# Kernel optimization log

Measured on AMD Instinct MI355X. Metric: run time of the kernel, lower is better.

Reference implementation:

```python
import jax, jax.numpy as jnp
import numpy as np

EPS = 1e-5
H, D = 8, 64  # n_heads, head_n_channels


def _instance_norm(x):
    # x: [B, H, N, D]; InstanceNorm1d over grid axis N per (batch, head, channel)
    m = jnp.mean(x, axis=2, keepdims=True)
    v = jnp.var(x, axis=2, keepdims=True)
    return (x - m) * jax.lax.rsqrt(v + EPS)


def setup_inputs() -> dict:
    key = jax.random.key(0)
    ks = jax.random.split(key, 7)
    B, N, C, OUT = 4, 16384, 256, 256
    u_src = jax.random.normal(ks[0], (B, N, C), jnp.float32)
    pos_src = jax.random.uniform(ks[1], (B, N, 2), jnp.float32)
    s_in = 1.0 / np.sqrt(C)
    Wq = jax.random.normal(ks[2], (H * D, C), jnp.float32) * s_in
    Wk = jax.random.normal(ks[3], (H * D, C), jnp.float32) * s_in
    Wv = jax.random.normal(ks[4], (H * D, C), jnp.float32) * s_in
    Wo = jax.random.normal(ks[5], (OUT, H * D), jnp.float32) * (1.0 / np.sqrt(H * D))
    bo = jnp.zeros((OUT,), jnp.float32)
    return {"u_src": u_src, "pos_src": pos_src, "Wq": Wq, "Wk": Wk, "Wv": Wv, "Wo": Wo, "bo": bo}


def reference(u_src, pos_src, Wq, Wk, Wv, Wo, bo):
    B, N, C = u_src.shape
    # q/k/v projections -> [B, H, N, D]
    q = (u_src @ Wq.T).reshape(B, N, H, D).transpose(0, 2, 1, 3)
    k = (u_src @ Wk.T).reshape(B, N, H, D).transpose(0, 2, 1, 3)
    v = (u_src @ Wv.T).reshape(B, N, H, D).transpose(0, 2, 1, 3)
    # instance-norm k, v over the grid (domain) axis
    k = _instance_norm(k)
    v = _instance_norm(v)
    # associative linear attention with uniform quadrature weights 1/N
    w = 1.0 / N
    kv = jnp.einsum('bhnd,bhne->bhde', k, v * w)   # [B,H,D,D]
    u = jnp.einsum('bhnd,bhde->bhne', q, kv)       # [B,H,N,D]
    u = u.transpose(0, 2, 1, 3).reshape(B, N, H * D)
    return u @ Wo.T + bo
```

## Files before the change

kernel.cpp:

```cpp
#include <hip/hip_runtime.h>
#include <hip/hip_bf16.h>

#define BB    4
#define NTOT  16384
#define CC    256
#define HH    8
#define DD    64
#define HD    512
#define OUTC  256

typedef unsigned short u16;
typedef unsigned int u32;
typedef __attribute__((ext_vector_type(8))) short bf16x8;
typedef __attribute__((ext_vector_type(4))) float f32x4;
typedef __attribute__((ext_vector_type(4))) short u16x4;
typedef __attribute__((ext_vector_type(4))) u32 u32x4;

__device__ __forceinline__ float b2f(u16 u) {
    union { float f; u32 i; } x; x.i = ((u32)u) << 16; return x.f;
}
__device__ __forceinline__ u16 f2b(float f) {
    union { float f; u32 i; } x; x.f = f;
    u32 r = x.i + 0x7fffu + ((x.i >> 16) & 1u);
    return (u16)(r >> 16);
}

#define GLD(gp, lp) __builtin_amdgcn_global_load_lds( \
    (const __attribute__((address_space(1))) void*)(gp), \
    (__attribute__((address_space(3))) void*)(lp), 16, 0, 0)

#define MFMA(a, b, c) __builtin_amdgcn_mfma_f32_16x16x32_bf16((a), (b), (c), 0, 0, 0)

__global__ __launch_bounds__(256) void wcvt(
    const float* __restrict__ Wq, const float* __restrict__ Wk,
    const float* __restrict__ Wv, const float* __restrict__ Wo,
    u16* __restrict__ q, u16* __restrict__ k,
    u16* __restrict__ v, u16* __restrict__ o)
{
    const int z = blockIdx.z;
    const float* src = z == 0 ? Wq : z == 1 ? Wk : z == 2 ? Wv : Wo;
    u16* dst = z == 0 ? q : z == 1 ? k : z == 2 ? v : o;
    const int i = (blockIdx.x * 256 + threadIdx.x) * 8;
    const float4 a = *(const float4*)(src + i);
    const float4 b = *(const float4*)(src + i + 4);
    union { bf16x8 v; u16 s[8]; } w;
    w.s[0] = f2b(a.x); w.s[1] = f2b(a.y); w.s[2] = f2b(a.z); w.s[3] = f2b(a.w);
    w.s[4] = f2b(b.x); w.s[5] = f2b(b.y); w.s[6] = f2b(b.z); w.s[7] = f2b(b.w);
    *(bf16x8*)(dst + i) = w.v;
}

__global__ __launch_bounds__(512) void ggemm(
    const float* __restrict__ u, float* __restrict__ Gp, float* __restrict__ suP,
    u16* __restrict__ u_b)
{
    __shared__ u32 Ts[16 * 290];
    const int z = blockIdx.x, b = z >> 6, ck = z & 63;
    const float* base = u + (long long)b * NTOT * CC + (long long)ck * 256 * CC;
    u16* ub_base = u_b + (long long)b * NTOT * CC + (long long)ck * 256 * CC;
    const int t = threadIdx.x, w = t >> 6, l = t & 63;
    const int wy = w >> 1, wx = w & 1;
    const int r16 = l & 15, quad = l >> 4;
    const int sp = t >> 5;
    const int sq = t & 31;

    const int csa0 = 9 * ((wy * 64 + r16) >> 3) + (r16 & 7);
    const int csb0 = 9 * ((wx * 128 + r16) >> 3) + (r16 & 7);
    const int pr0 = 4 * quad * 290;

    f32x4 acc[4][8] = {};
    float su = 0.f;

    float4 a0, a1, b0, b1;
    {
        const float* src = base + (long long)(2 * sp) * CC + sq * 8;
        a0 = *(const float4*)src;       a1 = *(const float4*)(src + 4);
        b0 = *(const float4*)(src + CC); b1 = *(const float4*)(src + CC + 4);
    }

    for (int it = 0; it < 8; it++) {
        __syncthreads();
        {
            union { bf16x8 v; u16 q[8]; } ra, rb;
            ra.q[0] = f2b(a0.x); ra.q[1] = f2b(a0.y); ra.q[2] = f2b(a0.z); ra.q[3] = f2b(a0.w);
            ra.q[4] = f2b(a1.x); ra.q[5] = f2b(a1.y); ra.q[6] = f2b(a1.z); ra.q[7] = f2b(a1.w);
            rb.q[0] = f2b(b0.x); rb.q[1] = f2b(b0.y); rb.q[2] = f2b(b0.z); rb.q[3] = f2b(b0.w);
            rb.q[4] = f2b(b1.x); rb.q[5] = f2b(b1.y); rb.q[6] = f2b(b1.z); rb.q[7] = f2b(b1.w);
            {
                u16* ub = ub_base + (long long)(it * 32 + 2 * sp) * CC + sq * 8;
                *(bf16x8*)ub = ra.v;
                *(bf16x8*)(ub + CC) = rb.v;
            }
            u32 pk[8];
#pragma unroll
            for (int k = 0; k < 8; k++)
                pk[k] = (u32)ra.q[k] | ((u32)rb.q[k] << 16);
            u32* dst = Ts + sp * 290 + 9 * sq;
#pragma unroll
            for (int k = 0; k < 8; k++) dst[k] = pk[k];
        }
        if (it < 7) {
            const float* src = base + (long long)((it + 1) * 32 + 2 * sp) * CC + sq * 8;
            a0 = *(const float4*)src;       a1 = *(const float4*)(src + 4);
            b0 = *(const float4*)(src + CC); b1 = *(const float4*)(src + CC + 4);
        }
        __syncthreads();

        if (t < 256) {
            const int cs = 9 * (t >> 3) + (t & 7);
            float s1 = 0.f;
#pragma unroll
            for (int p = 0; p < 16; p++) {
                u32 v = Ts[p * 290 + cs];
                s1 += b2f((u16)(v & 0xffff)) + b2f((u16)(v >> 16));
            }
            su += s1;
        }

        bf16x8 a[4], bb[8];
#pragma unroll
        for (int i = 0; i < 4; i++) {
            const int cs = csa0 + 18 * i;
            union { u32x4 u4; bf16x8 h; } f;
            f.u4[0] = Ts[pr0 + cs];       f.u4[1] = Ts[pr0 + 290 + cs];
            f.u4[2] = Ts[pr0 + 580 + cs]; f.u4[3] = Ts[pr0 + 870 + cs];
            a[i] = f.h;
        }
#pragma unroll
        for (int j = 0; j < 8; j++) {
            const int cs = csb0 + 18 * j;
            union { u32x4 u4; bf16x8 h; } f;
            f.u4[0] = Ts[pr0 + cs];       f.u4[1] = Ts[pr0 + 290 + cs];
            f.u4[2] = Ts[pr0 + 580 + cs]; f.u4[3] = Ts[pr0 + 870 + cs];
            bb[j] = f.h;
        }
#pragma unroll
        for (int i = 0; i < 4; i++)
#pragma unroll
            for (int j = 0; j < 8; j++)
                acc[i][j] = MFMA(a[i], bb[j], acc[i][j]);
    }

    float* Cp = Gp + (long long)z * 65536;
#pragma unroll
    for (int i = 0; i < 4; i++)
#pragma unroll
        for (int j = 0; j < 8; j++)
#pragma unroll
            for (int rr = 0; rr < 4; rr++)
                Cp[(wy * 64 + 16 * i + quad * 4 + rr) * 256 + wx * 128 + 16 * j + r16]
                    = acc[i][j][rr];
    if (t < 256) suP[z * 256 + t] = su;
}

__global__ __launch_bounds__(256) void gred(
    const float* __restrict__ Gp, const float* __restrict__ suP,
    u16* __restrict__ Gb, float* __restrict__ su)
{
    const int b = blockIdx.y, t = threadIdx.x;
    const int row = blockIdx.x * 4 + (t >> 6);
    const int col = (t & 63) * 4;
    const float* p = Gp + (long long)(b * 64) * 65536 + row * 256 + col;
    f32x4 s = {};
#pragma unroll
    for (int ck = 0; ck < 64; ck++) {
        f32x4 v = *(const f32x4*)(p + (long long)ck * 65536);
        s[0] += v[0]; s[1] += v[1]; s[2] += v[2]; s[3] += v[3];
    }
    union { u16x4 v; u16 q[4]; } pk;
#pragma unroll
    for (int k = 0; k < 4; k++) pk.q[k] = f2b(s[k]);
    *(u16x4*)(Gb + (long long)b * 65536 + row * 256 + col) = pk.v;

    if (blockIdx.x == 0) {
        float s2 = 0.f;
#pragma unroll
        for (int ck = 0; ck < 64; ck++) s2 += suP[(b * 64 + ck) * 256 + t];
        su[b * 256 + t] = s2;
    }
}

__global__ __launch_bounds__(256) void skvz(
    const u16* __restrict__ P2, const float* __restrict__ su,
    const u16* __restrict__ Wk_b, const u16* __restrict__ Wv_b,
    const u16* __restrict__ Wq_b, u16* __restrict__ Zt)
{
    __shared__ u16 pool[20480];
    __shared__ float mkL[64], rkL[64], mvL[64], rvL[64];

    const int bx = blockIdx.x, b = bx >> 3, h = bx & 7;
    const int t = threadIdx.x, w = t >> 6, l = t & 63;
    const int r16 = l & 15, quad = l >> 4;

    const u16* WkH = Wk_b + (h * 64) * 256;
    const u16* WvH = Wv_b + (h * 64) * 256;
    const u16* PkH = P2 + (long long)b * 262144 + (h * 64) * 256;
    const u16* PvH = P2 + (long long)b * 262144 + (512 + h * 64) * 256;

    {
        const int row = t >> 1, half = t & 1;
        const u16* Prow = (row < 64 ? PkH + row * 256 : PvH + (row - 64) * 256) + half * 128;
        const u16* Wrow = (row < 64 ? WkH + row * 256 : WvH + (row - 64) * 256) + half * 128;
        const float* suB = su + b * 256 + half * 128;
        float e2 = 0.f, m = 0.f;
#pragma unroll
        for (int c8 = 0; c8 < 16; c8++) {
            bf16x8 pw = *(const bf16x8*)(Prow + c8 * 8);
            bf16x8 ww = *(const bf16x8*)(Wrow + c8 * 8);
#pragma unroll
            for (int k = 0; k < 8; k++) {
                const float wv_ = b2f((u16)ww[k]);
                e2 += b2f((u16)pw[k]) * wv_;
                m  += wv_ * suB[c8 * 8 + k];
            }
        }
        e2 += __shfl_xor(e2, 1);
        m  += __shfl_xor(m, 1);
        if (half == 0) {
            m *= (1.0f / NTOT);
            const float r = rsqrtf(e2 * (1.0f / NTOT) - m * m + 1e-5f);
            if (row < 64) { mkL[row] = m; rkL[row] = r; }
            else          { mvL[row - 64] = m; rvL[row - 64] = r; }
        }
    }
    __syncthreads();

    const int mh = (w >> 1) * 32, nh = (w & 1) * 32;
    float mkR[2][4], rkR[2][4], mvR[2], rvR[2];
#pragma unroll
    for (int i = 0; i < 2; i++)
#pragma unroll
        for (int rr = 0; rr < 4; rr++) {
            mkR[i][rr] = mkL[mh + 16 * i + quad * 4 + rr];
            rkR[i][rr] = rkL[mh + 16 * i + quad * 4 + rr];
        }
#pragma unroll
    for (int j = 0; j < 2; j++) {
        mvR[j] = mvL[nh + 16 * j + r16];
        rvR[j] = rvL[nh + 16 * j + r16];
    }

    f32x4 accs[2][2] = {};
    for (int ch = 0; ch < 8; ch++) {
        const int ko = quad * 8;
        bf16x8 ap[2], bv[2];
#pragma unroll
        for (int i = 0; i < 2; i++)
            ap[i] = *(const bf16x8*)(PkH + (mh + 16 * i + r16) * 256 + ch * 32 + ko);
#pragma unroll
        for (int j = 0; j < 2; j++)
            bv[j] = *(const bf16x8*)(WvH + (nh + 16 * j + r16) * 256 + ch * 32 + ko);
#pragma unroll
        for (int i = 0; i < 2; i++)
#pragma unroll
            for (int j = 0; j < 2; j++)
                accs[i][j] = MFMA(ap[i], bv[j], accs[i][j]);
    }

    u16* kvTL = pool;
    u16* WqTL = pool + 4096;
#pragma unroll
    for (int i = 0; i < 2; i++)
#pragma unroll
        for (int j = 0; j < 2; j++)
#pragma unroll
            for (int rr = 0; rr < 4; rr++) {
                const int d = mh + 16 * i + quad * 4 + rr;
                const int e = nh + 16 * j + r16;
                const float kv = rkR[i][rr] * rvR[j] *
                    (accs[i][j][rr] * (1.0f / NTOT) - mkR[i][rr] * mvR[j]);
                kvTL[(d >> 5) * 2048 + e * 32 + (d & 31)] = f2b(kv);
            }
    {
        const int d = t >> 2, q = t & 3;
        const u16* Wrow = Wq_b + (h * 64 + d) * 256 + q * 64;
#pragma unroll
        for (int s = 0; s < 8; s++) {
            bf16x8 raw = *(const bf16x8*)(Wrow + s * 8);
#pragma unroll
            for (int k = 0; k < 8; k++) {
                const int c = q * 64 + s * 8 + k;
                WqTL[(d >> 5) * 8192 + c * 32 + (d & 31)] = (u16)raw[k];
            }
        }
    }
    __syncthreads();

    f32x4 accy[4][4] = {};
#pragma unroll
    for (int ch = 0; ch < 2; ch++) {
        const int ko = quad * 8;
        bf16x8 akv[4], bq[4];
#pragma unroll
        for (int i = 0; i < 4; i++)
            akv[i] = *(const bf16x8*)(kvTL + ch * 2048 + (16 * i + r16) * 32 + ko);
#pragma unroll
        for (int j = 0; j < 4; j++)
            bq[j] = *(const bf16x8*)(WqTL + ch * 8192 + (w * 64 + 16 * j + r16) * 32 + ko);
#pragma unroll
        for (int i = 0; i < 4; i++)
#pragma unroll
            for (int j = 0; j < 4; j++)
                accy[i][j] = MFMA(akv[i], bq[j], accy[i][j]);
    }
#pragma unroll
    for (int i = 0; i < 4; i++)
#pragma unroll
        for (int j = 0; j < 4; j++) {
            const int c = w * 64 + 16 * j + r16;
            const int e0 = 16 * i + quad * 4;
            union { u16x4 v; u16 s[4]; } pk;
#pragma unroll
            for (int rr = 0; rr < 4; rr++) pk.s[rr] = f2b(accy[i][j][rr]);
            *(u16x4*)(Zt + ((long long)(b * 256 + c)) * 512 + h * 64 + e0) = pk.v;
        }
}

template <typename CT>
__global__ __launch_bounds__(256) void gemm_bt(
    const u16* __restrict__ A, const u16* __restrict__ Bm,
    CT* __restrict__ C, const float* __restrict__ bias,
    int K, int lda, int ldc,
    long long aStride, long long bStride, long long cStride)
{
    __shared__ u16 As[128 * 32];
    __shared__ u16 Bs[128 * 32];

    const int bz = blockIdx.z;
    A  += (long long)bz * aStride;
    Bm += (long long)bz * bStride;
    C  += (long long)bz * cStride;

    const int m0 = blockIdx.x * 128;
    const int n0 = blockIdx.y * 128;
    const int t  = threadIdx.x;
    const int wv = t >> 6, l = t & 63;
    const int wy = wv >> 1, wx = wv & 1;
    const int r16  = l & 15;
    const int quad = l >> 4;
    const int srow = wv * 16 + (l >> 2);
    const int scol = (l & 3) * 8;

    f32x4 acc[4][4] = {};

    for (int kk = 0; kk < K; kk += 32) {
#pragma unroll
        for (int s = 0; s < 2; s++) {
            GLD(A + (long long)(m0 + s * 64 + srow) * lda + kk + scol,
                As + s * 2048 + wv * 512);
            GLD(Bm + (long long)(n0 + s * 64 + srow) * K + kk + scol,
                Bs + s * 2048 + wv * 512);
        }
        __syncthreads();

        bf16x8 a[4], b[4];
#pragma unroll
        for (int i = 0; i < 4; i++)
            a[i] = *(const bf16x8*)(As + (wy * 64 + 16 * i + r16) * 32 + quad * 8);
#pragma unroll
        for (int j = 0; j < 4; j++)
            b[j] = *(const bf16x8*)(Bs + (wx * 64 + 16 * j + r16) * 32 + quad * 8);
#pragma unroll
        for (int i = 0; i < 4; i++)
#pragma unroll
            for (int j = 0; j < 4; j++)
                acc[i][j] = MFMA(a[i], b[j], acc[i][j]);
        __syncthreads();
    }

#pragma unroll
    for (int j = 0; j < 4; j++) {
        const int col = n0 + wx * 64 + 16 * j + r16;
        const float bv = bias ? bias[col] : 0.0f;
#pragma unroll
        for (int i = 0; i < 4; i++) {
#pragma unroll
            for (int r = 0; r < 4; r++) {
                const int row = m0 + wy * 64 + 16 * i + quad * 4 + r;
                const float v = acc[i][j][r] + bv;
                if constexpr (sizeof(CT) == 2) C[(long long)row * ldc + col] = f2b(v);
                else                           C[(long long)row * ldc + col] = v;
            }
        }
    }
}

__global__ __launch_bounds__(256) void gemm_out(
    const u16* __restrict__ Au, const u16* __restrict__ Ft,
    float* __restrict__ C, const float* __restrict__ bias)
{
    __shared__ u16 As[128 * 32];
    __shared__ u16 Bs[256 * 32];

    const int b = blockIdx.z;
    Au += (long long)b * NTOT * CC;
    const u16* Bm = Ft + (long long)b * 65536;
    C += (long long)b * NTOT * OUTC;

    const int m0 = blockIdx.x * 128;
    const int t  = threadIdx.x;
    const int wv = t >> 6, l = t & 63;
    const int wy = wv >> 1, wx = wv & 1;
    const int r16  = l & 15;
    const int quad = l >> 4;
    const int srow = wv * 16 + (l >> 2);
    const int scol = (l & 3) * 8;

    f32x4 acc[4][8] = {};

    for (int kk = 0; kk < 256; kk += 32) {
#pragma unroll
        for (int s = 0; s < 2; s++)
            GLD(Au + (long long)(m0 + s * 64 + srow) * CC + kk + scol,
                As + s * 2048 + wv * 512);
#pragma unroll
        for (int s = 0; s < 4; s++)
            GLD(Bm + (long long)(s * 64 + srow) * 256 + kk + scol,
                Bs + s * 2048 + wv * 512);
        __syncthreads();

        bf16x8 a[4], bb[8];
#pragma unroll
        for (int i = 0; i < 4; i++)
            a[i] = *(const bf16x8*)(As + (wy * 64 + 16 * i + r16) * 32 + quad * 8);
#pragma unroll
        for (int j = 0; j < 8; j++)
            bb[j] = *(const bf16x8*)(Bs + (wx * 128 + 16 * j + r16) * 32 + quad * 8);
#pragma unroll
        for (int i = 0; i < 4; i++)
#pragma unroll
            for (int j = 0; j < 8; j++)
                acc[i][j] = MFMA(a[i], bb[j], acc[i][j]);
        __syncthreads();
    }

#pragma unroll
    for (int j = 0; j < 8; j++) {
        const int col = wx * 128 + 16 * j + r16;
        const float bv = bias[col];
#pragma unroll
        for (int i = 0; i < 4; i++) {
#pragma unroll
            for (int r = 0; r < 4; r++) {
                const int row = m0 + wy * 64 + 16 * i + quad * 4 + r;
                C[(long long)row * OUTC + col] = acc[i][j][r] + bv;
            }
        }
    }
}

extern "C" void kernel_launch(void* const* d_in, const int* in_sizes, int n_in,
                              void* d_out, int out_size, void* d_ws, size_t ws_size,
                              hipStream_t stream)
{
    const float* u_src = (const float*)d_in[0];
    const float* Wq = (const float*)d_in[2];
    const float* Wk = (const float*)d_in[3];
    const float* Wv = (const float*)d_in[4];
    const float* Wo = (const float*)d_in[5];
    const float* bo = (const float*)d_in[6];
    float* out = (float*)d_out;

    char* ws = (char*)d_ws;
    size_t off = 0;
    float* Gp  = (float*)(ws + off); off += 67108864;
    float* suP = (float*)(ws + off); off += 262144;
    u16*  Gb   = (u16*)(ws + off);  off += 524288;
    u16*  Wq_b = (u16*)(ws + off);  off += 262144;
    u16*  Wk_b = (u16*)(ws + off);  off += 262144;
    u16*  Wv_b = (u16*)(ws + off);  off += 262144;
    u16*  Wo_b = (u16*)(ws + off);  off += 262144;
    float* su  = (float*)(ws + off); off += 4096;
    u16*  Zt   = (u16*)(ws + off);  off += 1048576;
    u16*  Ft   = (u16*)(ws + off);  off += 524288;
    u16*  P2   = (u16*)(ws + off);  off += 2097152;
    u16*  u_b  = (u16*)(ws + off);  off += 33554432;

    const dim3 blk(256);

    wcvt<<<dim3(64, 1, 4), blk, 0, stream>>>(Wq, Wk, Wv, Wo, Wq_b, Wk_b, Wv_b, Wo_b);

    ggemm<<<dim3(BB * 64), dim3(512), 0, stream>>>(u_src, Gp, suP, u_b);
    gred<<<dim3(64, BB), blk, 0, stream>>>(Gp, suP, Gb, su);

    gemm_bt<u16><<<dim3(8, 2, BB), blk, 0, stream>>>(
        Wk_b, Gb, P2, nullptr, 256, 256, 256, 0, 65536, 262144);

    skvz<<<dim3(BB * HH), blk, 0, stream>>>(P2, su, Wk_b, Wv_b, Wq_b, Zt);

    gemm_bt<u16><<<dim3(2, 2, BB), blk, 0, stream>>>(
        Wo_b, Zt, Ft, nullptr, 512, 512, 256, 0, 131072, 65536);

    gemm_out<<<dim3(128, 1, BB), blk, 0, stream>>>(u_b, Ft, out, bo);
}
```

Before: 214.3 us.

## Double-buffer shared memory in GEMM kernels and move column sums to registers

Adds ping-pong LDS buffers to ggemm, gemm_bt and gemm_out so the next K-tile's global-to-LDS load is issued before the current tile's MFMAs. This drops one barrier per iteration and overlaps load latency with compute. In ggemm, the per-column sum is now accumulated in registers during bf16 conversion and reduced once through LDS at the end, replacing a per-iteration LDS sweep by half the threads. The cost is doubled LDS per block, which may lower occupancy.

```diff
diff --git a/kernel.cpp b/kernel.cpp
--- a/kernel.cpp
+++ b/kernel.cpp
@@ -53,7 +53,7 @@
     const float* __restrict__ u, float* __restrict__ Gp, float* __restrict__ suP,
     u16* __restrict__ u_b)
 {
-    __shared__ u32 Ts[16 * 290];
+    __shared__ u32 Ts[2 * 4640];
     const int z = blockIdx.x, b = z >> 6, ck = z & 63;
     const float* base = u + (long long)b * NTOT * CC + (long long)ck * 256 * CC;
     u16* ub_base = u_b + (long long)b * NTOT * CC + (long long)ck * 256 * CC;
@@ -68,7 +68,7 @@
     const int pr0 = 4 * quad * 290;
 
     f32x4 acc[4][8] = {};
-    float su = 0.f;
+    float su8[8] = {};
 
     float4 a0, a1, b0, b1;
     {
@@ -77,60 +77,54 @@
         b0 = *(const float4*)(src + CC); b1 = *(const float4*)(src + CC + 4);
     }
 
+    int cur = 0;
     for (int it = 0; it < 8; it++) {
-        __syncthreads();
+        const u32 coff = cur * 4640;
         {
             union { bf16x8 v; u16 q[8]; } ra, rb;
             ra.q[0] = f2b(a0.x); ra.q[1] = f2b(a0.y); ra.q[2] = f2b(a0.z); ra.q[3] = f2b(a0.w);
             ra.q[4] = f2b(a1.x); ra.q[5] = f2b(a1.y); ra.q[6] = f2b(a1.z); ra.q[7] = f2b(a1.w);
             rb.q[0] = f2b(b0.x); rb.q[1] = f2b(b0.y); rb.q[2] = f2b(b0.z); rb.q[3] = f2b(b0.w);
             rb.q[4] = f2b(b1.x); rb.q[5] = f2b(b1.y); rb.q[6] = f2b(b1.z); rb.q[7] = f2b(b1.w);
+#pragma unroll
+            for (int k = 0; k < 8; k++)
+                su8[k] += b2f(ra.q[k]) + b2f(rb.q[k]);
+            u32 pk[8];
+#pragma unroll
+            for (int k = 0; k < 8; k++)
+                pk[k] = (u32)ra.q[k] | ((u32)rb.q[k] << 16);
+            u32* dst = Ts + coff + sp * 290 + 9 * sq;
+#pragma unroll
+            for (int k = 0; k < 8; k++) dst[k] = pk[k];
             {
                 u16* ub = ub_base + (long long)(it * 32 + 2 * sp) * CC + sq * 8;
                 *(bf16x8*)ub = ra.v;
                 *(bf16x8*)(ub + CC) = rb.v;
             }
-            u32 pk[8];
-#pragma unroll
-            for (int k = 0; k < 8; k++)
-                pk[k] = (u32)ra.q[k] | ((u32)rb.q[k] << 16);
-            u32* dst = Ts + sp * 290 + 9 * sq;
-#pragma unroll
-            for (int k = 0; k < 8; k++) dst[k] = pk[k];
-        }
+        }
+        __syncthreads();
+
         if (it < 7) {
             const float* src = base + (long long)((it + 1) * 32 + 2 * sp) * CC + sq * 8;
             a0 = *(const float4*)src;       a1 = *(const float4*)(src + 4);
             b0 = *(const float4*)(src + CC); b1 = *(const float4*)(src + CC + 4);
         }
-        __syncthreads();
-
-        if (t < 256) {
-            const int cs = 9 * (t >> 3) + (t & 7);
-            float s1 = 0.f;
-#pragma unroll
-            for (int p = 0; p < 16; p++) {
-                u32 v = Ts[p * 290 + cs];
-                s1 += b2f((u16)(v & 0xffff)) + b2f((u16)(v >> 16));
-            }
-            su += s1;
-        }
 
         bf16x8 a[4], bb[8];
 #pragma unroll
         for (int i = 0; i < 4; i++) {
-            const int cs = csa0 + 18 * i;
+            const int cs = coff + pr0 + csa0 + 18 * i;
             union { u32x4 u4; bf16x8 h; } f;
-            f.u4[0] = Ts[pr0 + cs];       f.u4[1] = Ts[pr0 + 290 + cs];
-            f.u4[2] = Ts[pr0 + 580 + cs]; f.u4[3] = Ts[pr0 + 870 + cs];
+            f.u4[0] = Ts[cs];       f.u4[1] = Ts[290 + cs];
+            f.u4[2] = Ts[580 + cs]; f.u4[3] = Ts[870 + cs];
             a[i] = f.h;
         }
 #pragma unroll
         for (int j = 0; j < 8; j++) {
-            const int cs = csb0 + 18 * j;
+            const int cs = coff + pr0 + csb0 + 18 * j;
             union { u32x4 u4; bf16x8 h; } f;
-            f.u4[0] = Ts[pr0 + cs];       f.u4[1] = Ts[pr0 + 290 + cs];
-            f.u4[2] = Ts[pr0 + 580 + cs]; f.u4[3] = Ts[pr0 + 870 + cs];
+            f.u4[0] = Ts[cs];       f.u4[1] = Ts[290 + cs];
+            f.u4[2] = Ts[580 + cs]; f.u4[3] = Ts[870 + cs];
             bb[j] = f.h;
         }
 #pragma unroll
@@ -138,6 +132,7 @@
 #pragma unroll
             for (int j = 0; j < 8; j++)
                 acc[i][j] = MFMA(a[i], bb[j], acc[i][j]);
+        cur ^= 1;
     }
 
     float* Cp = Gp + (long long)z * 65536;
@@ -149,7 +144,18 @@
             for (int rr = 0; rr < 4; rr++)
                 Cp[(wy * 64 + 16 * i + quad * 4 + rr) * 256 + wx * 128 + 16 * j + r16]
                     = acc[i][j][rr];
-    if (t < 256) suP[z * 256 + t] = su;
+
+    __syncthreads();
+    float* S = (float*)Ts;
+#pragma unroll
+    for (int k = 0; k < 8; k++) S[sp * 264 + sq * 8 + k] = su8[k];
+    __syncthreads();
+    if (t < 256) {
+        float s = 0.f;
+#pragma unroll
+        for (int p = 0; p < 16; p++) s += S[p * 264 + t];
+        suP[z * 256 + t] = s;
+    }
 }
 
 __global__ __launch_bounds__(256) void gred(
@@ -322,8 +328,8 @@
     int K, int lda, int ldc,
     long long aStride, long long bStride, long long cStride)
 {
-    __shared__ u16 As[128 * 32];
-    __shared__ u16 Bs[128 * 32];
+    __shared__ u16 As[2][128 * 32];
+    __shared__ u16 Bs[2][128 * 32];
 
     const int bz = blockIdx.z;
     A  += (long long)bz * aStride;
@@ -340,31 +346,38 @@
     const int srow = wv * 16 + (l >> 2);
     const int scol = (l & 3) * 8;
 
-    f32x4 acc[4][4] = {};
-
-    for (int kk = 0; kk < K; kk += 32) {
+    auto stage = [&](int kk, int buf) {
 #pragma unroll
         for (int s = 0; s < 2; s++) {
             GLD(A + (long long)(m0 + s * 64 + srow) * lda + kk + scol,
-                As + s * 2048 + wv * 512);
+                As[buf] + s * 2048 + wv * 512);
             GLD(Bm + (long long)(n0 + s * 64 + srow) * K + kk + scol,
-                Bs + s * 2048 + wv * 512);
-        }
-        __syncthreads();
+                Bs[buf] + s * 2048 + wv * 512);
+        }
+    };
+
+    f32x4 acc[4][4] = {};
+
+    stage(0, 0);
+    __syncthreads();
+    int cur = 0;
+    for (int kk = 0; kk < K; kk += 32) {
+        if (kk + 32 < K) stage(kk + 32, cur ^ 1);
 
         bf16x8 a[4], b[4];
 #pragma unroll
         for (int i = 0; i < 4; i++)
-            a[i] = *(const bf16x8*)(As + (wy * 64 + 16 * i + r16) * 32 + quad * 8);
+            a[i] = *(const bf16x8*)(As[cur] + (wy * 64 + 16 * i + r16) * 32 + quad * 8);
 #pragma unroll
         for (int j = 0; j < 4; j++)
-            b[j] = *(const bf16x8*)(Bs + (wx * 64 + 16 * j + r16) * 32 + quad * 8);
+            b[j] = *(const bf16x8*)(Bs[cur] + (wx * 64 + 16 * j + r16) * 32 + quad * 8);
 #pragma unroll
         for (int i = 0; i < 4; i++)
 #pragma unroll
             for (int j = 0; j < 4; j++)
                 acc[i][j] = MFMA(a[i], b[j], acc[i][j]);
         __syncthreads();
+        cur ^= 1;
     }
 
 #pragma unroll
@@ -388,8 +401,8 @@
     const u16* __restrict__ Au, const u16* __restrict__ Ft,
     float* __restrict__ C, const float* __restrict__ bias)
 {
-    __shared__ u16 As[128 * 32];
-    __shared__ u16 Bs[256 * 32];
+    __shared__ u16 As[2][128 * 32];
+    __shared__ u16 Bs[2][256 * 32];
 
     const int b = blockIdx.z;
     Au += (long long)b * NTOT * CC;
@@ -405,32 +418,39 @@
     const int srow = wv * 16 + (l >> 2);
     const int scol = (l & 3) * 8;
 
-    f32x4 acc[4][8] = {};
-
-    for (int kk = 0; kk < 256; kk += 32) {
+    auto stage = [&](int kk, int buf) {
 #pragma unroll
         for (int s = 0; s < 2; s++)
             GLD(Au + (long long)(m0 + s * 64 + srow) * CC + kk + scol,
-                As + s * 2048 + wv * 512);
+                As[buf] + s * 2048 + wv * 512);
 #pragma unroll
         for (int s = 0; s < 4; s++)
             GLD(Bm + (long long)(s * 64 + srow) * 256 + kk + scol,
-                Bs + s * 2048 + wv * 512);
-        __syncthreads();
+                Bs[buf] + s * 2048 + wv * 512);
+    };
+
+    f32x4 acc[4][8] = {};
+
+    stage(0, 0);
+    __syncthreads();
+    int cur = 0;
+    for (int kk = 0; kk < 256; kk += 32) {
+        if (kk + 32 < 256) stage(kk + 32, cur ^ 1);
 
         bf16x8 a[4], bb[8];
 #pragma unroll
         for (int i = 0; i < 4; i++)
-            a[i] = *(const bf16x8*)(As + (wy * 64 + 16 * i + r16) * 32 + quad * 8);
+            a[i] = *(const bf16x8*)(As[cur] + (wy * 64 + 16 * i + r16) * 32 + quad * 8);
 #pragma unroll
         for (int j = 0; j < 8; j++)
-            bb[j] = *(const bf16x8*)(Bs + (wx * 128 + 16 * j + r16) * 32 + quad * 8);
+            bb[j] = *(const bf16x8*)(Bs[cur] + (wx * 128 + 16 * j + r16) * 32 + quad * 8);
 #pragma unroll
         for (int i = 0; i < 4; i++)
 #pragma unroll
             for (int j = 0; j < 8; j++)
                 acc[i][j] = MFMA(a[i], bb[j], acc[i][j]);
         __syncthreads();
+        cur ^= 1;
     }
 
 #pragma unroll
```

Measured after the change: 219.5 us. 1.02x slower.
